# Kernel optimization log

Measured on AMD Instinct MI355X. Metric: run time of the kernel, lower is better.

The kernel has to match this reference:

```python
import jax, jax.numpy as jnp
import numpy as np

N = 100000
E = 1000000
IN_C, HID, OUT_C = 128, 128, 40
DROPOUT_P = 0.5
BN_EPS = 1e-5


def setup_inputs() -> dict:
    key = jax.random.key(0)
    ks = jax.random.split(key, 10)
    x = jax.random.normal(ks[0], (N, IN_C), dtype=jnp.float32)
    edge_index = jax.random.randint(ks[1], (2, E), 0, N, dtype=jnp.int32)

    def glorot(k, fan_in, fan_out):
        lim = np.sqrt(6.0 / (fan_in + fan_out)).astype(np.float32)
        return jax.random.uniform(k, (fan_in, fan_out), jnp.float32, -lim, lim)

    return {
        "x": x,
        "edge_index": edge_index,
        "W1": glorot(ks[2], IN_C, HID), "b1": jnp.zeros((HID,), jnp.float32),
        "g1": jnp.ones((HID,), jnp.float32), "be1": jnp.zeros((HID,), jnp.float32),
        "W2": glorot(ks[3], HID, HID), "b2": jnp.zeros((HID,), jnp.float32),
        "g2": jnp.ones((HID,), jnp.float32), "be2": jnp.zeros((HID,), jnp.float32),
        "W3": glorot(ks[4], HID, OUT_C), "b3": jnp.zeros((OUT_C,), jnp.float32),
    }


def _deg_inv_sqrt(dst):
    # degree from destination nodes, +1 for the added self loop (PyG gcn_norm)
    deg = jax.ops.segment_sum(jnp.ones((E,), jnp.float32), dst, num_segments=N) + 1.0
    return jax.lax.rsqrt(deg)


def _gcn_conv(h, W, b, src, dst, dinv):
    # h: [N, Cin] -> [N, Cout]; y = D^-1/2 (A + I) D^-1/2 (h W) + b
    hw = h @ W
    norm = dinv[src] * dinv[dst]                      # [E]
    msg = hw[src] * norm[:, None]                     # [E, Cout] gather (memory-bound)
    agg = jax.ops.segment_sum(msg, dst, num_segments=N)
    agg = agg + hw * (dinv * dinv)[:, None]           # self-loop contribution
    return agg + b


def _batchnorm(h, gamma, beta):
    mu = jnp.mean(h, axis=0)
    var = jnp.mean(jnp.square(h - mu), axis=0)        # biased, training mode
    return (h - mu) * jax.lax.rsqrt(var + BN_EPS) * gamma + beta


def _dropout(h, key):
    keep = jax.random.bernoulli(key, 1.0 - DROPOUT_P, h.shape)
    return jnp.where(keep, h / (1.0 - DROPOUT_P), 0.0)


def reference(x, edge_index, W1, b1, g1, be1, W2, b2, g2, be2, W3, b3):
    src, dst = edge_index[0], edge_index[1]
    dinv = _deg_inv_sqrt(dst)
    dk = jax.random.split(jax.random.key(42), 2)

    h = _gcn_conv(x, W1, b1, src, dst, dinv)
    h = _dropout(jax.nn.relu(_batchnorm(h, g1, be1)), dk[0])

    h = _gcn_conv(h, W2, b2, src, dst, dinv)
    h = _dropout(jax.nn.relu(_batchnorm(h, g2, be2)), dk[1])

    h = _gcn_conv(h, W3, b3, src, dst, dinv)
    return jax.nn.log_softmax(h, axis=1)
```

## Files before the change

### kernel.cpp

```cpp
#include <hip/hip_runtime.h>
#include <math.h>

typedef __attribute__((ext_vector_type(8))) short bf16x8;
typedef __attribute__((ext_vector_type(4))) float f32x4;

__device__ __forceinline__ float bfbits2f(unsigned short b){
  return __uint_as_float(((unsigned)b) << 16);
}
__device__ __forceinline__ unsigned short f2bfbits(float f){
  unsigned u = __float_as_uint(f);
  unsigned r = u + 0x7fffu + ((u >> 16) & 1u);
  return (unsigned short)(r >> 16);
}

__host__ __device__ __forceinline__ unsigned rotl32(unsigned v, int d){
  return (v << d) | (v >> (32 - d));
}
__host__ __device__ __forceinline__ void tf2x32(unsigned k0, unsigned k1,
                                                unsigned c0, unsigned c1,
                                                unsigned &o0, unsigned &o1)
{
  unsigned ks2 = k0 ^ k1 ^ 0x1BD11BDAu;
  unsigned x0 = c0 + k0, x1 = c1 + k1;
#define TFR(r) x0 += x1; x1 = rotl32(x1, r); x1 ^= x0;
  TFR(13) TFR(15) TFR(26) TFR(6)
  x0 += k1;  x1 += ks2 + 1u;
  TFR(17) TFR(29) TFR(16) TFR(24)
  x0 += ks2; x1 += k0 + 2u;
  TFR(13) TFR(15) TFR(26) TFR(6)
  x0 += k0;  x1 += k1 + 3u;
  TFR(17) TFR(29) TFR(16) TFR(24)
  x0 += k1;  x1 += ks2 + 4u;
  TFR(13) TFR(15) TFR(26) TFR(6)
  x0 += ks2; x1 += k0 + 5u;
#undef TFR
  o0 = x0; o1 = x1;
}

__global__ __launch_bounds__(256) void k_countpos(const int* __restrict__ dst,
                                                  int* __restrict__ cnt,
                                                  int* __restrict__ pos, int E)
{
  int g = blockIdx.x * 256 + threadIdx.x;
  int base = g * 4;
  if (base + 3 < E){
    int4 d = ((const int4*)dst)[g];
    int4 p;
    p.x = atomicAdd(&cnt[d.x], 1);
    p.y = atomicAdd(&cnt[d.y], 1);
    p.z = atomicAdd(&cnt[d.z], 1);
    p.w = atomicAdd(&cnt[d.w], 1);
    ((int4*)pos)[g] = p;
  } else {
    for (int j = 0; j < 4; j++){
      int e = base + j;
      if (e < E) pos[e] = atomicAdd(&cnt[dst[e]], 1);
    }
  }
}

__global__ __launch_bounds__(256) void k_blocksum(const int* __restrict__ cnt,
                                                  int* __restrict__ bsum, int N)
{
  __shared__ int sh[256];
  int t = threadIdx.x;
  int base = blockIdx.x * 1024 + t * 4;
  int s = 0;
  #pragma unroll
  for (int j = 0; j < 4; j++){ int i = base + j; if (i < N) s += cnt[i]; }
  sh[t] = s; __syncthreads();
  for (int off = 128; off; off >>= 1){
    if (t < off) sh[t] += sh[t + off];
    __syncthreads();
  }
  if (t == 0) bsum[blockIdx.x] = sh[0];
}

__global__ __launch_bounds__(256) void k_scansums(const int* __restrict__ bsum,
                                                  int* __restrict__ boff,
                                                  int* __restrict__ rowstart,
                                                  int NB, int N)
{
  __shared__ int sh[256];
  int t = threadIdx.x;
  int v = (t < NB) ? bsum[t] : 0;
  sh[t] = v; __syncthreads();
  for (int off = 1; off < 256; off <<= 1){
    int x = sh[t];
    int y = (t >= off) ? sh[t - off] : 0;
    __syncthreads();
    sh[t] = x + y;
    __syncthreads();
  }
  if (t < NB) boff[t] = sh[t] - v;
  if (t == NB - 1) rowstart[N] = sh[t];
}

__global__ __launch_bounds__(256) void k_scanfinal(const int* __restrict__ cnt,
                                                   const int* __restrict__ boff,
                                                   int* __restrict__ rowstart,
                                                   float* __restrict__ dinv, int N)
{
  __shared__ int sh[256];
  int t = threadIdx.x;
  int base = blockIdx.x * 1024 + t * 4;
  int c0 = 0, c1 = 0, c2 = 0, c3 = 0;
  if (base + 0 < N) c0 = cnt[base + 0];
  if (base + 1 < N) c1 = cnt[base + 1];
  if (base + 2 < N) c2 = cnt[base + 2];
  if (base + 3 < N) c3 = cnt[base + 3];
  int s = c0 + c1 + c2 + c3;
  sh[t] = s; __syncthreads();
  for (int off = 1; off < 256; off <<= 1){
    int x = sh[t];
    int y = (t >= off) ? sh[t - off] : 0;
    __syncthreads();
    sh[t] = x + y;
    __syncthreads();
  }
  int excl = sh[t] - s + boff[blockIdx.x];
  if (base + 0 < N){ rowstart[base+0] = excl;          dinv[base+0] = rsqrtf((float)c0 + 1.f); }
  if (base + 1 < N){ rowstart[base+1] = excl+c0;       dinv[base+1] = rsqrtf((float)c1 + 1.f); }
  if (base + 2 < N){ rowstart[base+2] = excl+c0+c1;    dinv[base+2] = rsqrtf((float)c2 + 1.f); }
  if (base + 3 < N){ rowstart[base+3] = excl+c0+c1+c2; dinv[base+3] = rsqrtf((float)c3 + 1.f); }
}

__global__ __launch_bounds__(256) void k_fill(const int* __restrict__ src,
                                              const int* __restrict__ dst,
                                              const int* __restrict__ pos,
                                              const int* __restrict__ rowstart,
                                              int* __restrict__ csr, int E)
{
  int g = blockIdx.x * 256 + threadIdx.x;
  int base = g * 4;
  if (base + 3 < E){
    int4 d = ((const int4*)dst)[g];
    int4 p = ((const int4*)pos)[g];
    int4 s = ((const int4*)src)[g];
    int r0 = rowstart[d.x], r1 = rowstart[d.y], r2 = rowstart[d.z], r3 = rowstart[d.w];
    csr[r0 + p.x] = s.x;
    csr[r1 + p.y] = s.y;
    csr[r2 + p.z] = s.z;
    csr[r3 + p.w] = s.w;
  } else {
    for (int j = 0; j < 4; j++){
      int e = base + j;
      if (e < E) csr[rowstart[dst[e]] + pos[e]] = src[e];
    }
  }
}

__global__ __launch_bounds__(256) void k_wt(const float* __restrict__ W1,
                                            const float* __restrict__ W2,
                                            const float* __restrict__ W3,
                                            unsigned short* __restrict__ WT1,
                                            unsigned short* __restrict__ WT2,
                                            unsigned short* __restrict__ WT3)
{
  const float* W; unsigned short* WT; int Cout, Cpad;
  if (blockIdx.x == 0){ W = W1; WT = WT1; Cout = 128; Cpad = 128; }
  else if (blockIdx.x == 1){ W = W2; WT = WT2; Cout = 128; Cpad = 128; }
  else { W = W3; WT = WT3; Cout = 40; Cpad = 48; }
  int tot = Cpad * 128;
  for (int i = threadIdx.x; i < tot; i += 256){
    int n = i >> 7, k = i & 127;
    float v = (n < Cout) ? W[k * Cout + n] : 0.f;
    WT[i] = f2bfbits(v);
  }
}

template<int NT, int MODE>
__global__ __launch_bounds__(256) void k_gemm_mfma(const void* __restrict__ Ap,
                                                   const unsigned short* __restrict__ WT,
                                                   const float* __restrict__ dinv,
                                                   const float* __restrict__ stats,
                                                   const float* __restrict__ g,
                                                   const float* __restrict__ be,
                                                   unsigned k0, unsigned k1, float invN,
                                                   unsigned short* __restrict__ outb,
                                                   int N, int Cout)
{
  __shared__ uint4 Wl4[NT * 16 * 16];
  __shared__ uint4 Al4[64 * 16];
  __shared__ float bnS[128], bnB[128];
  const int t = threadIdx.x;
  const int w = t >> 6, l = t & 63;
  const long rb0 = (long)blockIdx.x * 64;
  const int wrow0 = w * 16;

  uint4 rawU[4];
  float4 rawF[4][2];
  int rr[4], cc[4];
  bool inr[4];
  #pragma unroll
  for (int i = 0; i < 4; i++){
    int idx = i * 64 + l;
    int r = idx >> 4, c = idx & 15;
    long grow = rb0 + wrow0 + r;
    rr[i] = r; cc[i] = c; inr[i] = (grow < N);
    if (inr[i]){
      if (MODE == 0){
        const float* ap = (const float*)Ap + grow * 128 + c * 8;
        rawF[i][0] = *(const float4*)ap;
        rawF[i][1] = *(const float4*)(ap + 4);
      } else {
        rawU[i] = *(const uint4*)((const unsigned short*)Ap + grow * 128 + c * 8);
      }
    }
  }

  {
    const uint4* s4 = (const uint4*)WT;
    const int tot = NT * 16 * 16;
    for (int i = t; i < tot; i += 256){
      int n = i >> 4, c = i & 15;
      Wl4[n * 16 + (c ^ (n & 15))] = s4[i];
    }
  }
  if (MODE == 2 && t < 128){
    float ss = 0.f, qq = 0.f;
    #pragma unroll
    for (int i = 0; i < 16; i++){
      ss += stats[i * 256 + t];
      qq += stats[i * 256 + 128 + t];
    }
    float mean = ss * invN;
    float var = fmaxf(qq * invN - mean * mean, 0.f);
    float rstd = rsqrtf(var + 1e-5f);
    float sc = g[t] * rstd;
    bnS[t] = sc;
    bnB[t] = be[t] - mean * sc;
  }
  __syncthreads();

  #pragma unroll
  for (int i = 0; i < 4; i++){
    uint4 chunk = make_uint4(0u, 0u, 0u, 0u);
    if (inr[i]){
      if (MODE == 0){
        chunk.x = (unsigned)f2bfbits(rawF[i][0].x) | ((unsigned)f2bfbits(rawF[i][0].y) << 16);
        chunk.y = (unsigned)f2bfbits(rawF[i][0].z) | ((unsigned)f2bfbits(rawF[i][0].w) << 16);
        chunk.z = (unsigned)f2bfbits(rawF[i][1].x) | ((unsigned)f2bfbits(rawF[i][1].y) << 16);
        chunk.w = (unsigned)f2bfbits(rawF[i][1].z) | ((unsigned)f2bfbits(rawF[i][1].w) << 16);
      } else {
        long grow = rb0 + wrow0 + rr[i];
        unsigned idxb = (unsigned)grow * 128u + (unsigned)(cc[i] * 8);
        const unsigned* rw = &rawU[i].x;
        unsigned* cw = &chunk.x;
        #pragma unroll
        for (int h = 0; h < 4; h++){
          int ch = cc[i] * 8 + 2 * h;
          float f0 = bfbits2f((unsigned short)(rw[h] & 0xffffu));
          float f1 = bfbits2f((unsigned short)(rw[h] >> 16));
          f0 = fmaxf(fmaf(f0, bnS[ch],     bnB[ch]),     0.f);
          f1 = fmaxf(fmaf(f1, bnS[ch + 1], bnB[ch + 1]), 0.f);
          unsigned w0, w1;
          tf2x32(k0, k1, 0u, idxb + 2u * h,      w0, w1);
          f0 = ((w0 ^ w1) & 0x80000000u) ? 0.f : f0 * 2.f;
          tf2x32(k0, k1, 0u, idxb + 2u * h + 1u, w0, w1);
          f1 = ((w0 ^ w1) & 0x80000000u) ? 0.f : f1 * 2.f;
          cw[h] = (unsigned)f2bfbits(f0) | ((unsigned)f2bfbits(f1) << 16);
        }
      }
    }
    Al4[(wrow0 + rr[i]) * 16 + (cc[i] ^ rr[i])] = chunk;
  }

  const int lm = l & 15, q = l >> 4;

  f32x4 acc[NT];
  #pragma unroll
  for (int nt = 0; nt < NT; nt++){
    acc[nt][0] = 0.f; acc[nt][1] = 0.f; acc[nt][2] = 0.f; acc[nt][3] = 0.f;
  }

  #pragma unroll
  for (int kt = 0; kt < 4; kt++){
    const int x = kt * 4 + q;
    bf16x8 a = *(const bf16x8*)&Al4[(wrow0 + lm) * 16 + (x ^ lm)];
    #pragma unroll
    for (int nt = 0; nt < NT; nt++){
      int brow = nt * 16 + lm;
      bf16x8 b = *(const bf16x8*)&Wl4[brow * 16 + (x ^ (brow & 15))];
      acc[nt] = __builtin_amdgcn_mfma_f32_16x16x32_bf16(a, b, acc[nt], 0, 0, 0);
    }
  }

  #pragma unroll
  for (int r = 0; r < 4; r++){
    long row = rb0 + wrow0 + q * 4 + r;
    if (row < N){
      float dv = dinv[row];
      #pragma unroll
      for (int nt = 0; nt < NT; nt++){
        int col = nt * 16 + lm;
        if (col < Cout)
          outb[row * Cout + col] = f2bfbits(acc[nt][r] * dv);
      }
    }
  }
}

#define ACC8(U) do{ uint4 _u = (U); \
  a0 += bfbits2f((unsigned short)(_u.x & 0xffffu)); \
  a1 += bfbits2f((unsigned short)(_u.x >> 16)); \
  a2 += bfbits2f((unsigned short)(_u.y & 0xffffu)); \
  a3 += bfbits2f((unsigned short)(_u.y >> 16)); \
  a4 += bfbits2f((unsigned short)(_u.z & 0xffffu)); \
  a5 += bfbits2f((unsigned short)(_u.z >> 16)); \
  a6 += bfbits2f((unsigned short)(_u.w & 0xffffu)); \
  a7 += bfbits2f((unsigned short)(_u.w >> 16)); }while(0)

__global__ __launch_bounds__(256) void k_agg128s(const unsigned short* __restrict__ hw,
                                                 const int* __restrict__ rs,
                                                 const int* __restrict__ csr,
                                                 const float* __restrict__ dinv,
                                                 unsigned short* __restrict__ outb,
                                                 float* __restrict__ stats,
                                                 int N)
{
  const int l = threadIdx.x;
  const int ns = l >> 4;
  const int sl = l & 15;
  const int ty = threadIdx.y;
  const int grp = ty * 4 + ns;
  const uint4* h16 = (const uint4*)hw;
  const int base = blockIdx.x * 32;

  float s0=0.f,s1=0.f,s2=0.f,s3=0.f,s4=0.f,s5=0.f,s6=0.f,s7=0.f;
  float q0=0.f,q1=0.f,q2=0.f,q3=0.f,q4=0.f,q5=0.f,q6=0.f,q7=0.f;

  #pragma unroll 1
  for (int it = 0; it < 2; it++){
    int v = base + it * 16 + grp;
    if (v < N){
      float a0=0.f,a1=0.f,a2=0.f,a3=0.f,a4=0.f,a5=0.f,a6=0.f,a7=0.f;
      ACC8(h16[(size_t)v * 16 + sl]);
      int e0 = rs[v], e1 = rs[v + 1];
      int i = e0;
      for (; i + 4 <= e1; i += 4){
        int sa = csr[i], sb = csr[i+1], sc = csr[i+2], sd = csr[i+3];
        uint4 m0 = h16[(size_t)sa * 16 + sl];
        uint4 m1 = h16[(size_t)sb * 16 + sl];
        uint4 m2 = h16[(size_t)sc * 16 + sl];
        uint4 m3 = h16[(size_t)sd * 16 + sl];
        ACC8(m0); ACC8(m1); ACC8(m2); ACC8(m3);
      }
      for (; i < e1; i++){
        ACC8(h16[(size_t)csr[i] * 16 + sl]);
      }
      float dv = dinv[v];
      a0*=dv; a1*=dv; a2*=dv; a3*=dv; a4*=dv; a5*=dv; a6*=dv; a7*=dv;
      uint4 o;
      o.x = (unsigned)f2bfbits(a0) | ((unsigned)f2bfbits(a1) << 16);
      o.y = (unsigned)f2bfbits(a2) | ((unsigned)f2bfbits(a3) << 16);
      o.z = (unsigned)f2bfbits(a4) | ((unsigned)f2bfbits(a5) << 16);
      o.w = (unsigned)f2bfbits(a6) | ((unsigned)f2bfbits(a7) << 16);
      ((uint4*)outb)[(size_t)v * 16 + sl] = o;
      s0+=a0; q0=fmaf(a0,a0,q0);  s1+=a1; q1=fmaf(a1,a1,q1);
      s2+=a2; q2=fmaf(a2,a2,q2);  s3+=a3; q3=fmaf(a3,a3,q3);
      s4+=a4; q4=fmaf(a4,a4,q4);  s5+=a5; q5=fmaf(a5,a5,q5);
      s6+=a6; q6=fmaf(a6,a6,q6);  s7+=a7; q7=fmaf(a7,a7,q7);
    }
  }

  __shared__ float shS[16][128], shQ[16][128];
  *(float4*)&shS[grp][sl * 8]     = make_float4(s0, s1, s2, s3);
  *(float4*)&shS[grp][sl * 8 + 4] = make_float4(s4, s5, s6, s7);
  *(float4*)&shQ[grp][sl * 8]     = make_float4(q0, q1, q2, q3);
  *(float4*)&shQ[grp][sl * 8 + 4] = make_float4(q4, q5, q6, q7);
  __syncthreads();
  int t = ty * 64 + threadIdx.x;
  if (t < 128){
    float ss = 0.f, qq = 0.f;
    #pragma unroll
    for (int g2 = 0; g2 < 16; g2++){ ss += shS[g2][t]; qq += shQ[g2][t]; }
    float* dstat = stats + (blockIdx.x & 15) * 256;
    atomicAdd(&dstat[t], ss);
    atomicAdd(&dstat[128 + t], qq);
  }
}

#define ACC2(U) do{ unsigned _u = (U); \
  acx += bfbits2f((unsigned short)(_u & 0xffffu)); \
  acy += bfbits2f((unsigned short)(_u >> 16)); }while(0)

__global__ __launch_bounds__(256) void k_agg40lsm(const unsigned short* __restrict__ hw,
                                                  const int* __restrict__ rs,
                                                  const int* __restrict__ csr,
                                                  const float* __restrict__ dinv,
                                                  const float* __restrict__ b3,
                                                  float* __restrict__ out, int N)
{
  int half = (threadIdx.x >> 5) & 1;
  int sl = threadIdx.x & 31;
  int v = blockIdx.x * 8 + threadIdx.y * 2 + half;
  bool nact = (v < N);
  bool act = nact && (sl < 20);
  const unsigned* h2 = (const unsigned*)hw;
  float acx = 0.f, acy = 0.f, dv = 1.f;
  if (act){
    dv = dinv[v];
    ACC2(h2[(size_t)v * 20 + sl]);
    int e0 = rs[v], e1 = rs[v + 1];
    int i = e0;
    for (; i + 4 <= e1; i += 4){
      int s0 = csr[i], s1 = csr[i+1], s2 = csr[i+2], s3 = csr[i+3];
      unsigned u0 = h2[(size_t)s0 * 20 + sl];
      unsigned u1 = h2[(size_t)s1 * 20 + sl];
      unsigned u2 = h2[(size_t)s2 * 20 + sl];
      unsigned u3 = h2[(size_t)s3 * 20 + sl];
      ACC2(u0); ACC2(u1); ACC2(u2); ACC2(u3);
    }
    for (; i < e1; i++){
      ACC2(h2[(size_t)csr[i] * 20 + sl]);
    }
  }
  float x0 = act ? fmaf(acx, dv, b3[2 * sl])     : -INFINITY;
  float x1 = act ? fmaf(acy, dv, b3[2 * sl + 1]) : -INFINITY;
  float m = fmaxf(x0, x1);
  #pragma unroll
  for (int off = 16; off; off >>= 1) m = fmaxf(m, __shfl_xor(m, off, 32));
  float e = act ? (expf(x0 - m) + expf(x1 - m)) : 0.f;
  #pragma unroll
  for (int off = 16; off; off >>= 1) e += __shfl_xor(e, off, 32);
  float lse = m + logf(e);
  if (act){
    float2 o; o.x = x0 - lse; o.y = x1 - lse;
    *reinterpret_cast<float2*>(out + (size_t)v * 40 + 2 * sl) = o;
  }
}

extern "C" void kernel_launch(void* const* d_in, const int* in_sizes, int n_in,
                              void* d_out, int out_size, void* d_ws, size_t ws_size,
                              hipStream_t stream)
{
  const float* x  = (const float*)d_in[0];
  const int* ei   = (const int*)d_in[1];
  const float* W1 = (const float*)d_in[2];
  const float* g1 = (const float*)d_in[4];
  const float* be1= (const float*)d_in[5];
  const float* W2 = (const float*)d_in[6];
  const float* g2 = (const float*)d_in[8];
  const float* be2= (const float*)d_in[9];
  const float* W3 = (const float*)d_in[10];
  const float* b3 = (const float*)d_in[11];
  float* out = (float*)d_out;

  const int N = in_sizes[0] / 128;
  const int E = in_sizes[1] / 2;
  const int* srcv = ei;
  const int* dstv = ei + E;

  char* ws = (char*)d_ws;
  size_t off = 0;
  auto take = [&](size_t bytes) -> void* {
    void* p = ws + off;
    off = (off + bytes + 255) & ~(size_t)255;
    return p;
  };
  int*   cnt      = (int*)  take((size_t)N * 4);
  int*   pos      = (int*)  take((size_t)E * 4);
  int*   rowstart = (int*)  take((size_t)(N + 1) * 4);
  int*   csr      = (int*)  take((size_t)E * 4);
  float* dinv     = (float*)take((size_t)N * 4);
  int*   bsum     = (int*)  take(256 * 4);
  int*   boff     = (int*)  take(256 * 4);
  float* stats    = (float*)take(16 * 256 * 4);
  unsigned short* WT1 = (unsigned short*)take(128 * 128 * 2);
  unsigned short* WT2 = (unsigned short*)take(128 * 128 * 2);
  unsigned short* WT3 = (unsigned short*)take(48 * 128 * 2);
  unsigned short* bufX = (unsigned short*)take((size_t)N * 128 * 2);
  unsigned short* bufY = (unsigned short*)take((size_t)N * 128 * 2);
  (void)ws_size; (void)n_in; (void)out_size;

  unsigned l1k0, l1k1, l2k0, l2k1;
  tf2x32(0u, 42u, 0u, 0u, l1k0, l1k1);
  tf2x32(0u, 42u, 0u, 1u, l2k0, l2k1);

  const float invN = 1.0f / (float)N;
  const int NB = (N + 1023) / 1024;
  dim3 wgrid8((N + 7) / 8), wblk(64, 4);
  dim3 wgrid32((N + 31) / 32);
  const int ggrid = (N + 63) / 64;
  const int egrid = (E + 1023) / 1024;

  hipMemsetAsync(cnt, 0, (size_t)N * 4, stream);
  k_countpos<<<egrid, 256, 0, stream>>>(dstv, cnt, pos, E);
  k_blocksum<<<NB, 256, 0, stream>>>(cnt, bsum, N);
  k_scansums<<<1, 256, 0, stream>>>(bsum, boff, rowstart, NB, N);
  k_scanfinal<<<NB, 256, 0, stream>>>(cnt, boff, rowstart, dinv, N);
  k_fill<<<egrid, 256, 0, stream>>>(srcv, dstv, pos, rowstart, csr, E);
  k_wt<<<3, 256, 0, stream>>>(W1, W2, W3, WT1, WT2, WT3);

  k_gemm_mfma<8, 0><<<ggrid, 256, 0, stream>>>(x, WT1, dinv,
      nullptr, nullptr, nullptr, 0u, 0u, invN, bufX, N, 128);
  hipMemsetAsync(stats, 0, 16 * 256 * 4, stream);
  k_agg128s<<<wgrid32, wblk, 0, stream>>>(bufX, rowstart, csr, dinv, bufY, stats, N);

  k_gemm_mfma<8, 2><<<ggrid, 256, 0, stream>>>(bufY, WT2, dinv,
      stats, g1, be1, l1k0, l1k1, invN, bufX, N, 128);
  hipMemsetAsync(stats, 0, 16 * 256 * 4, stream);
  k_agg128s<<<wgrid32, wblk, 0, stream>>>(bufX, rowstart, csr, dinv, bufY, stats, N);

  k_gemm_mfma<3, 2><<<ggrid, 256, 0, stream>>>(bufY, WT3, dinv,
      stats, g2, be2, l2k0, l2k1, invN, bufX, N, 40);
  k_agg40lsm<<<wgrid8, wblk, 0, stream>>>(bufX, rowstart, csr, dinv, b3, out, N);
}
```

Baseline: 418.9 us.

## Precompute dropout bitmasks in preprocessing kernels instead of inside GEMM

```diff
diff --git a/kernel.cpp b/kernel.cpp
--- a/kernel.cpp
+++ b/kernel.cpp
@@ -37,9 +37,27 @@
   o0 = x0; o1 = x1;
 }
 
+__device__ __forceinline__ void gen_mask(unsigned* __restrict__ mask,
+                                         unsigned mk0, unsigned mk1,
+                                         int g, int total, int M)
+{
+  for (int wi = g; wi < M; wi += total){
+    unsigned bits = 0u;
+    #pragma unroll 4
+    for (int j = 0; j < 32; j++){
+      unsigned w0, w1;
+      tf2x32(mk0, mk1, 0u, (unsigned)wi * 32u + (unsigned)j, w0, w1);
+      bits |= (((w0 ^ w1) >> 31) << j);
+    }
+    mask[wi] = bits;
+  }
+}
+
 __global__ __launch_bounds__(256) void k_countpos(const int* __restrict__ dst,
                                                   int* __restrict__ cnt,
-                                                  int* __restrict__ pos, int E)
+                                                  int* __restrict__ pos, int E,
+                                                  unsigned* __restrict__ mask,
+                                                  unsigned mk0, unsigned mk1, int M)
 {
   int g = blockIdx.x * 256 + threadIdx.x;
   int base = g * 4;
@@ -57,6 +75,7 @@
       if (e < E) pos[e] = atomicAdd(&cnt[dst[e]], 1);
     }
   }
+  gen_mask(mask, mk0, mk1, g, gridDim.x * 256, M);
 }
 
 __global__ __launch_bounds__(256) void k_blocksum(const int* __restrict__ cnt,
@@ -129,7 +148,9 @@
                                               const int* __restrict__ dst,
                                               const int* __restrict__ pos,
                                               const int* __restrict__ rowstart,
-                                              int* __restrict__ csr, int E)
+                                              int* __restrict__ csr, int E,
+                                              unsigned* __restrict__ mask,
+                                              unsigned mk0, unsigned mk1, int M)
 {
   int g = blockIdx.x * 256 + threadIdx.x;
   int base = g * 4;
@@ -148,6 +169,7 @@
       if (e < E) csr[rowstart[dst[e]] + pos[e]] = src[e];
     }
   }
+  gen_mask(mask, mk0, mk1, g, gridDim.x * 256, M);
 }
 
 __global__ __launch_bounds__(256) void k_wt(const float* __restrict__ W1,
@@ -176,7 +198,8 @@
                                                    const float* __restrict__ stats,
                                                    const float* __restrict__ g,
                                                    const float* __restrict__ be,
-                                                   unsigned k0, unsigned k1, float invN,
+                                                   const unsigned* __restrict__ mask,
+                                                   float invN,
                                                    unsigned short* __restrict__ outb,
                                                    int N, int Cout)
 {
@@ -190,6 +213,7 @@
 
   uint4 rawU[4];
   float4 rawF[4][2];
+  unsigned mword[4];
   int rr[4], cc[4];
   bool inr[4];
   #pragma unroll
@@ -205,6 +229,7 @@
         rawF[i][1] = *(const float4*)(ap + 4);
       } else {
         rawU[i] = *(const uint4*)((const unsigned short*)Ap + grow * 128 + c * 8);
+        mword[i] = mask[((unsigned)grow << 2) + (c >> 2)];
       }
     }
   }
@@ -243,8 +268,7 @@
         chunk.z = (unsigned)f2bfbits(rawF[i][1].x) | ((unsigned)f2bfbits(rawF[i][1].y) << 16);
         chunk.w = (unsigned)f2bfbits(rawF[i][1].z) | ((unsigned)f2bfbits(rawF[i][1].w) << 16);
       } else {
-        long grow = rb0 + wrow0 + rr[i];
-        unsigned idxb = (unsigned)grow * 128u + (unsigned)(cc[i] * 8);
+        unsigned mb = mword[i] >> ((cc[i] & 3) * 8);
         const unsigned* rw = &rawU[i].x;
         unsigned* cw = &chunk.x;
         #pragma unroll
@@ -254,11 +278,8 @@
           float f1 = bfbits2f((unsigned short)(rw[h] >> 16));
           f0 = fmaxf(fmaf(f0, bnS[ch],     bnB[ch]),     0.f);
           f1 = fmaxf(fmaf(f1, bnS[ch + 1], bnB[ch + 1]), 0.f);
-          unsigned w0, w1;
-          tf2x32(k0, k1, 0u, idxb + 2u * h,      w0, w1);
-          f0 = ((w0 ^ w1) & 0x80000000u) ? 0.f : f0 * 2.f;
-          tf2x32(k0, k1, 0u, idxb + 2u * h + 1u, w0, w1);
-          f1 = ((w0 ^ w1) & 0x80000000u) ? 0.f : f1 * 2.f;
+          f0 = ((mb >> (2 * h))     & 1u) ? 0.f : f0 * 2.f;
+          f1 = ((mb >> (2 * h + 1)) & 1u) ? 0.f : f1 * 2.f;
           cw[h] = (unsigned)f2bfbits(f0) | ((unsigned)f2bfbits(f1) << 16);
         }
       }
@@ -467,6 +488,8 @@
   int*   bsum     = (int*)  take(256 * 4);
   int*   boff     = (int*)  take(256 * 4);
   float* stats    = (float*)take(16 * 256 * 4);
+  unsigned* mask1 = (unsigned*)take((size_t)N * 4 * 4);
+  unsigned* mask2 = (unsigned*)take((size_t)N * 4 * 4);
   unsigned short* WT1 = (unsigned short*)take(128 * 128 * 2);
   unsigned short* WT2 = (unsigned short*)take(128 * 128 * 2);
   unsigned short* WT3 = (unsigned short*)take(48 * 128 * 2);
@@ -479,6 +502,7 @@
   tf2x32(0u, 42u, 0u, 1u, l2k0, l2k1);
 
   const float invN = 1.0f / (float)N;
+  const int M = N * 4;
   const int NB = (N + 1023) / 1024;
   dim3 wgrid8((N + 7) / 8), wblk(64, 4);
   dim3 wgrid32((N + 31) / 32);
@@ -486,24 +510,24 @@
   const int egrid = (E + 1023) / 1024;
 
   hipMemsetAsync(cnt, 0, (size_t)N * 4, stream);
-  k_countpos<<<egrid, 256, 0, stream>>>(dstv, cnt, pos, E);
+  k_countpos<<<egrid, 256, 0, stream>>>(dstv, cnt, pos, E, mask1, l1k0, l1k1, M);
   k_blocksum<<<NB, 256, 0, stream>>>(cnt, bsum, N);
   k_scansums<<<1, 256, 0, stream>>>(bsum, boff, rowstart, NB, N);
   k_scanfinal<<<NB, 256, 0, stream>>>(cnt, boff, rowstart, dinv, N);
-  k_fill<<<egrid, 256, 0, stream>>>(srcv, dstv, pos, rowstart, csr, E);
+  k_fill<<<egrid, 256, 0, stream>>>(srcv, dstv, pos, rowstart, csr, E, mask2, l2k0, l2k1, M);
   k_wt<<<3, 256, 0, stream>>>(W1, W2, W3, WT1, WT2, WT3);
 
   k_gemm_mfma<8, 0><<<ggrid, 256, 0, stream>>>(x, WT1, dinv,
-      nullptr, nullptr, nullptr, 0u, 0u, invN, bufX, N, 128);
+      nullptr, nullptr, nullptr, nullptr, invN, bufX, N, 128);
   hipMemsetAsync(stats, 0, 16 * 256 * 4, stream);
   k_agg128s<<<wgrid32, wblk, 0, stream>>>(bufX, rowstart, csr, dinv, bufY, stats, N);
 
   k_gemm_mfma<8, 2><<<ggrid, 256, 0, stream>>>(bufY, WT2, dinv,
-      stats, g1, be1, l1k0, l1k1, invN, bufX, N, 128);
+      stats, g1, be1, mask1, invN, bufX, N, 128);
   hipMemsetAsync(stats, 0, 16 * 256 * 4, stream);
   k_agg128s<<<wgrid32, wblk, 0, stream>>>(bufX, rowstart, csr, dinv, bufY, stats, N);
 
   k_gemm_mfma<3, 2><<<ggrid, 256, 0, stream>>>(bufY, WT3, dinv,
-      stats, g2, be2, l2k0, l2k1, invN, bufX, N, 40);
+      stats, g2, be2, mask2, invN, bufX, N, 40);
   k_agg40lsm<<<wgrid8, wblk, 0, stream>>>(bufX, rowstart, csr, dinv, b3, out, N);
 }
```

Measured after the change: 415.6 us. Within noise of the previous version (-0.8%).
